# Kernel tuning notes

Measured on AMD Instinct MI355X. Metric: run time of the kernel, lower is better.

The kernel has to match this reference:

```python
import jax, jax.numpy as jnp
import numpy as np

NC1, NC2 = 97, 300   # EPIC-Kitchens verb / noun class counts
T_FRAMES = 24000     # frames in one long video
N_ACTIONS = 3806     # (verb, noun) action pairs in mapping.txt
HID = 512            # cfg.hid_dim


def setup_inputs() -> dict:
    key = jax.random.key(0)
    k1, k2, k3 = jax.random.split(key, 3)
    H = HID + NC1 + NC2  # 909: hidden features with class logits appended
    frame_feature = jax.random.normal(k1, (T_FRAMES, 1, H), dtype=jnp.float32)
    vids = jax.random.randint(k2, (N_ACTIONS,), 0, NC1, dtype=jnp.int32)
    nids = jax.random.randint(k3, (N_ACTIONS,), 0, NC2, dtype=jnp.int32)
    return {"frame_feature": frame_feature, "vids": vids, "nids": nids}


def _combine_verb_noun(clogit, vids, nids):
    # combine_verb_noun_to_action with apply_log=True:
    # log_softmax verbs and nouns separately, gather per action id, add.
    vlog = jax.nn.log_softmax(clogit[..., :NC1], axis=-1)
    nlog = jax.nn.log_softmax(clogit[..., NC1:], axis=-1)
    return vlog[..., vids] + nlog[..., nids]


def reference(frame_feature, vids, nids):
    T = frame_feature.shape[0]
    # --- verb/noun softmax-gather-multiply combine (frame level) ---
    clogit = frame_feature[..., -NC1 - NC2:]                 # [T,1,NC1+NC2]
    frame_logp = _combine_verb_noun(clogit, vids, nids)      # [T,1,A]

    # --- parse_label: segment ids from per-frame argmax prediction ---
    pred = jnp.argmax(frame_logp[:, 0], axis=-1)             # [T]
    change = jnp.concatenate(
        [jnp.zeros((1,), jnp.int32), (pred[1:] != pred[:-1]).astype(jnp.int32)]
    )
    seg_id = jax.lax.stop_gradient(jnp.cumsum(change))       # [T], in [0, nseg)

    # --- TemporalDownsampleUpsample.feature_frame2seg: mean-pool per segment ---
    feat = frame_feature[:, 0]                               # [T,H]
    seg_sum = jax.ops.segment_sum(feat, seg_id, num_segments=T)
    cnt = jax.ops.segment_sum(jnp.ones((T, 1), feat.dtype), seg_id, num_segments=T)
    seg_feat = seg_sum / jnp.maximum(cnt, 1.0)               # [T,H] (padded segments)

    # segment-level verb/noun combine
    seg_logp = _combine_verb_noun(seg_feat[:, -NC1 - NC2:], vids, nids)  # [T,A]

    # --- feature_seg2frame: broadcast segment values back to frames ---
    s2f = seg_logp[seg_id]                                   # [T,A]
    return frame_logp + s2f[:, None, :]                      # [T,1,A]
```

## Files before the change

### kernel.cpp

```cpp
#include <hip/hip_runtime.h>
#include <math.h>

#define T_FRAMES 24000
#define NC1 97
#define NC2 300
#define NCC 397
#define NA 3806
#define NA_PAD 3808
#define H_DIM 909
#define COFF 512
#define SLG_STRIDE 400


__device__ __forceinline__ float waveMax(float v) {
#pragma unroll
    for (int off = 32; off > 0; off >>= 1) v = fmaxf(v, __shfl_xor(v, off));
    return v;
}

__device__ __forceinline__ float waveSum(float v) {
#pragma unroll
    for (int off = 32; off > 0; off >>= 1) v += __shfl_xor(v, off);
    return v;
}

__device__ __forceinline__ unsigned flip32(float f) {
    unsigned u = __float_as_uint(f);
    return (u & 0x80000000u) ? ~u : (u | 0x80000000u);
}


__global__ __launch_bounds__(256) void k_pack(const int* __restrict__ vids,
                                              const int* __restrict__ nids,
                                              int* __restrict__ pk) {
    int a = blockIdx.x * 256 + threadIdx.x;
    if (a < NA_PAD) pk[a] = (a < NA) ? (vids[a] | (nids[a] << 16)) : 0;
}


__global__ __launch_bounds__(256) void k_frame(const float* __restrict__ ff,
                                               const int* __restrict__ pk,
                                               float2* __restrict__ fstats,
                                               int* __restrict__ pred) {
    const int tid = threadIdx.x;
    const int wid = tid >> 6, lane = tid & 63;
    const int t = blockIdx.x * 4 + wid;

    __shared__ float sh[4][SLG_STRIDE];
    float* S = sh[wid];

    const float* row = ff + (size_t)t * H_DIM + COFF;

    float xv[7];
    float vmax = -INFINITY, nmax = -INFINITY;
#pragma unroll
    for (int j = 0; j < 7; j++) {
        const int idx = lane + j * 64;
        float x = -INFINITY;
        if (idx < NCC) { x = row[idx]; S[idx] = x; }
        xv[j] = x;
        if (idx < NC1) vmax = fmaxf(vmax, x);
        else           nmax = fmaxf(nmax, x);
    }
    vmax = waveMax(vmax);
    nmax = waveMax(nmax);

    float vs = 0.f, ns = 0.f;
#pragma unroll
    for (int j = 0; j < 7; j++) {
        const int idx = lane + j * 64;
        if (idx < NC1)      vs += __expf(xv[j] - vmax);
        else if (idx < NCC) ns += __expf(xv[j] - nmax);
    }
    vs = waveSum(vs);
    ns = waveSum(ns);
    const float c1 = vmax + __logf(vs);
    const float c2 = nmax + __logf(ns);

    const int4* pk4 = (const int4*)pk;
    unsigned long long best = 0ull;
    for (int g = lane; g < NA_PAD / 4; g += 64) {
        const int4 p4 = pk4[g];
        const int pv[4] = {p4.x, p4.y, p4.z, p4.w};
#pragma unroll
        for (int j = 0; j < 4; j++) {
            const int a = g * 4 + j;
            if (a < NA) {
                const int p = pv[j];
                const float val = S[p & 0xffff] + S[NC1 + (p >> 16)];
                const unsigned long long key =
                    ((unsigned long long)flip32(val) << 32) | (unsigned)(~(unsigned)a);
                best = (key > best) ? key : best;
            }
        }
    }
#pragma unroll
    for (int off = 32; off > 0; off >>= 1) {
        unsigned long long o = __shfl_xor(best, off);
        best = (o > best) ? o : best;
    }

    if (lane == 0) {
        pred[t] = (int)(~(unsigned)best);
        fstats[t] = make_float2(c1, c2);
    }
}


__global__ __launch_bounds__(1024) void k_scan(const int* __restrict__ pred,
                                               int* __restrict__ seg_id,
                                               int* __restrict__ seg_start,
                                               int* __restrict__ Scount) {
    const int tid = threadIdx.x;
    __shared__ unsigned short sid16[T_FRAMES];
    __shared__ int wsum[16];

    for (int t = tid; t < T_FRAMES; t += 1024) {
        int chg = (t > 0) ? (pred[t] != pred[t - 1]) : 0;
        sid16[t] = (unsigned short)chg;
    }
    __syncthreads();

    const int CH = (T_FRAMES + 1023) / 1024;
    const int base = tid * CH;
    int cnt = 0;
    for (int k = 0; k < CH; k++) {
        int t = base + k;
        if (t < T_FRAMES) cnt += sid16[t];
    }
    const int lane = tid & 63, wid = tid >> 6;
    int inc = cnt;
#pragma unroll
    for (int d = 1; d < 64; d <<= 1) {
        int n = __shfl_up(inc, d);
        if (lane >= d) inc += n;
    }
    if (lane == 63) wsum[wid] = inc;
    __syncthreads();
    if (tid == 0) {
        int acc = 0;
        for (int i = 0; i < 16; i++) { int x = wsum[i]; wsum[i] = acc; acc += x; }
    }
    __syncthreads();
    int sid = wsum[wid] + inc - cnt;

    for (int k = 0; k < CH; k++) {
        int t = base + k;
        if (t >= T_FRAMES) break;
        if (t == 0) {
            seg_start[0] = 0;
        } else if (sid16[t]) {
            sid++;
            seg_start[sid] = t;
        }
        sid16[t] = (unsigned short)sid;
        if (t == T_FRAMES - 1) *Scount = sid + 1;
    }
    __syncthreads();

    for (int t = tid; t < T_FRAMES; t += 1024) seg_id[t] = (int)sid16[t];
}


__global__ __launch_bounds__(256) void k_seg(const float* __restrict__ ff,
                                             const int* __restrict__ seg_start,
                                             const int* __restrict__ Scount,
                                             float* __restrict__ seg_lg) {
    const int tid = threadIdx.x;
    const int wid = tid >> 6, lane = tid & 63;
    const int s = blockIdx.x * 4 + wid;
    const int S = *Scount;
    if (s >= S) return;

    const int start = seg_start[s];
    const int end = (s + 1 < S) ? seg_start[s + 1] : T_FRAMES;
    const int len = end - start;

    float acc[7] = {0.f, 0.f, 0.f, 0.f, 0.f, 0.f, 0.f};
    const float* basep = ff + (size_t)start * H_DIM + COFF;
    for (int k = 0; k < len; k++) {
        const float* p = basep + (size_t)k * H_DIM;
#pragma unroll
        for (int j = 0; j < 7; j++) {
            const int idx = lane + j * 64;
            if (idx < NCC) acc[j] += p[idx];
        }
    }
    const float inv = 1.f / (float)len;

    float xv[7];
    float vmax = -INFINITY, nmax = -INFINITY;
#pragma unroll
    for (int j = 0; j < 7; j++) {
        const int idx = lane + j * 64;
        float x = (idx < NCC) ? acc[j] * inv : -INFINITY;
        xv[j] = x;
        if (idx < NC1) vmax = fmaxf(vmax, x);
        else           nmax = fmaxf(nmax, x);
    }
    vmax = waveMax(vmax);
    nmax = waveMax(nmax);

    float vs = 0.f, ns = 0.f;
#pragma unroll
    for (int j = 0; j < 7; j++) {
        const int idx = lane + j * 64;
        if (idx < NC1)      vs += __expf(xv[j] - vmax);
        else if (idx < NCC) ns += __expf(xv[j] - nmax);
    }
    vs = waveSum(vs);
    ns = waveSum(ns);
    const float lv = __logf(vs), ln_ = __logf(ns);

    float* dst = seg_lg + (size_t)s * SLG_STRIDE;
#pragma unroll
    for (int j = 0; j < 7; j++) {
        const int idx = lane + j * 64;
        if (idx < NCC)
            dst[idx] = (idx < NC1) ? ((xv[j] - vmax) - lv) : ((xv[j] - nmax) - ln_);
    }
}


__global__ __launch_bounds__(256) void k_out(const float* __restrict__ ff,
                                             const int* __restrict__ pk,
                                             const float2* __restrict__ fstats,
                                             const int* __restrict__ seg_id,
                                             const float* __restrict__ seg_lg,
                                             float* __restrict__ out) {
    const int tid = threadIdx.x;
    const int wid = tid >> 6, lane = tid & 63;
    const int t = blockIdx.x * 4 + wid;

    __shared__ float sh[4][SLG_STRIDE];
    float* S = sh[wid];

    const int s = seg_id[t];
    const float2 c = fstats[t];
    const float* row = ff + (size_t)t * H_DIM + COFF;
    const float* srow = seg_lg + (size_t)s * SLG_STRIDE;

#pragma unroll
    for (int j = 0; j < 7; j++) {
        const int idx = lane + j * 64;
        if (idx < NCC)
            S[idx] = row[idx] + srow[idx] - ((idx < NC1) ? c.x : c.y);
    }

    const int2* pk2 = (const int2*)pk;
    float* orow = out + (size_t)t * NA;
    for (int g = lane; g < NA / 2; g += 64) {
        const int2 p2 = pk2[g];
        float2 o;
        o.x = S[p2.x & 0xffff] + S[NC1 + (p2.x >> 16)];
        o.y = S[p2.y & 0xffff] + S[NC1 + (p2.y >> 16)];
        *(float2*)(orow + 2 * g) = o;
    }
}


extern "C" void kernel_launch(void* const* d_in, const int* in_sizes, int n_in,
                              void* d_out, int out_size, void* d_ws, size_t ws_size,
                              hipStream_t stream) {
    const float* ff = (const float*)d_in[0];
    const int* vids = (const int*)d_in[1];
    const int* nids = (const int*)d_in[2];
    float* out = (float*)d_out;

    char* ws = (char*)d_ws;
    size_t off = 0;
    float2* fstats = (float2*)(ws + off); off += (size_t)T_FRAMES * 8;
    int* pred = (int*)(ws + off);         off += (size_t)T_FRAMES * 4;
    int* seg_id = (int*)(ws + off);       off += (size_t)T_FRAMES * 4;
    int* seg_start = (int*)(ws + off);    off += (size_t)T_FRAMES * 4;
    int* Scount = (int*)(ws + off);       off += 16;
    int* pk = (int*)(ws + off);           off += (size_t)NA_PAD * 4;
    float* seg_lg = (float*)(ws + off);   off += (size_t)T_FRAMES * SLG_STRIDE * 4;

    k_pack<<<(NA_PAD + 255) / 256, 256, 0, stream>>>(vids, nids, pk);
    k_frame<<<T_FRAMES / 4, 256, 0, stream>>>(ff, pk, fstats, pred);
    k_scan<<<1, 1024, 0, stream>>>(pred, seg_id, seg_start, Scount);
    k_seg<<<T_FRAMES / 4, 256, 0, stream>>>(ff, seg_start, Scount, seg_lg);
    k_out<<<T_FRAMES / 4, 256, 0, stream>>>(ff, pk, fstats, seg_id, seg_lg, out);
}
```

Before: 551.0 us.

## Fuse segment pooling with output writes and sort action keys by noun

Result: faster. 521.3 us (-5.4%).

```diff
diff --git a/kernel.cpp b/kernel.cpp
--- a/kernel.cpp
+++ b/kernel.cpp
@@ -7,9 +7,10 @@
 #define NCC 397
 #define NA 3806
 #define NA_PAD 3808
+#define NSORT 4096
 #define H_DIM 909
 #define COFF 512
-#define SLG_STRIDE 400
+#define TAB 400
 
 
 __device__ __forceinline__ float waveMax(float v) {
@@ -30,23 +31,59 @@
 }
 
 
-__global__ __launch_bounds__(256) void k_pack(const int* __restrict__ vids,
+__global__ __launch_bounds__(256) void k_prep(const int* __restrict__ vids,
                                               const int* __restrict__ nids,
-                                              int* __restrict__ pk) {
-    int a = blockIdx.x * 256 + threadIdx.x;
-    if (a < NA_PAD) pk[a] = (a < NA) ? (vids[a] | (nids[a] << 16)) : 0;
+                                              int* __restrict__ pk,
+                                              unsigned* __restrict__ skey) {
+    __shared__ unsigned cnt[NC2];
+    __shared__ unsigned ofs[NC2];
+    const int tid = threadIdx.x;
+
+    for (int i = tid; i < NC2; i += 256) cnt[i] = 0u;
+    __syncthreads();
+
+    for (int a = tid; a < NA; a += 256) {
+        int v = vids[a], n = nids[a];
+        pk[a] = v | (n << 16);
+        atomicAdd(&cnt[n], 1u);
+    }
+    __syncthreads();
+
+    if (tid < 64) {
+        unsigned run = 0;
+        for (int c = 0; c < 5; c++) {
+            int i = c * 64 + tid;
+            unsigned x = (i < NC2) ? cnt[i] : 0u;
+            unsigned inc = x;
+#pragma unroll
+            for (int d = 1; d < 64; d <<= 1) {
+                unsigned y = __shfl_up(inc, d);
+                if (tid >= d) inc += y;
+            }
+            if (i < NC2) ofs[i] = run + inc - x;
+            run += __shfl(inc, 63);
+        }
+    }
+    __syncthreads();
+
+    for (int a = tid; a < NA; a += 256) {
+        unsigned v = (unsigned)vids[a], n = (unsigned)nids[a];
+        unsigned p = atomicAdd(&ofs[n], 1u);
+        skey[p] = (n << 19) | (v << 12) | (unsigned)a;
+    }
+    for (int i = NA + tid; i < NSORT; i += 256) skey[i] = 0xFFFFFFFFu;
 }
 
 
 __global__ __launch_bounds__(256) void k_frame(const float* __restrict__ ff,
-                                               const int* __restrict__ pk,
+                                               const unsigned* __restrict__ skey,
                                                float2* __restrict__ fstats,
                                                int* __restrict__ pred) {
     const int tid = threadIdx.x;
     const int wid = tid >> 6, lane = tid & 63;
     const int t = blockIdx.x * 4 + wid;
 
-    __shared__ float sh[4][SLG_STRIDE];
+    __shared__ float sh[4][TAB];
     float* S = sh[wid];
 
     const float* row = ff + (size_t)t * H_DIM + COFF;
@@ -77,20 +114,19 @@
     const float c1 = vmax + __logf(vs);
     const float c2 = nmax + __logf(ns);
 
-    const int4* pk4 = (const int4*)pk;
+    const uint4* sk4 = (const uint4*)skey;
     unsigned long long best = 0ull;
-    for (int g = lane; g < NA_PAD / 4; g += 64) {
-        const int4 p4 = pk4[g];
-        const int pv[4] = {p4.x, p4.y, p4.z, p4.w};
+    for (int g = lane; g < NSORT / 4; g += 64) {
+        const uint4 kq = sk4[g];
+        const unsigned ks[4] = {kq.x, kq.y, kq.z, kq.w};
 #pragma unroll
         for (int j = 0; j < 4; j++) {
-            const int a = g * 4 + j;
-            if (a < NA) {
-                const int p = pv[j];
-                const float val = S[p & 0xffff] + S[NC1 + (p >> 16)];
-                const unsigned long long key =
-                    ((unsigned long long)flip32(val) << 32) | (unsigned)(~(unsigned)a);
-                best = (key > best) ? key : best;
+            const unsigned kk = ks[j];
+            if (kk != 0xFFFFFFFFu) {
+                const float val = S[(kk >> 12) & 0x7Fu] + S[NC1 + (kk >> 19)];
+                const unsigned long long rk =
+                    ((unsigned long long)flip32(val) << 32) | ((~kk) & 0xFFFu);
+                best = (rk > best) ? rk : best;
             }
         }
     }
@@ -101,24 +137,21 @@
     }
 
     if (lane == 0) {
-        pred[t] = (int)(~(unsigned)best);
+        pred[t] = (int)((~(unsigned)best) & 0xFFFu);
         fstats[t] = make_float2(c1, c2);
     }
 }
 
 
 __global__ __launch_bounds__(1024) void k_scan(const int* __restrict__ pred,
-                                               int* __restrict__ seg_id,
                                                int* __restrict__ seg_start,
                                                int* __restrict__ Scount) {
     const int tid = threadIdx.x;
-    __shared__ unsigned short sid16[T_FRAMES];
+    __shared__ unsigned short flg[T_FRAMES];
     __shared__ int wsum[16];
 
-    for (int t = tid; t < T_FRAMES; t += 1024) {
-        int chg = (t > 0) ? (pred[t] != pred[t - 1]) : 0;
-        sid16[t] = (unsigned short)chg;
-    }
+    for (int t = tid; t < T_FRAMES; t += 1024)
+        flg[t] = (unsigned short)((t > 0) ? (pred[t] != pred[t - 1]) : 0);
     __syncthreads();
 
     const int CH = (T_FRAMES + 1023) / 1024;
@@ -126,7 +159,7 @@
     int cnt = 0;
     for (int k = 0; k < CH; k++) {
         int t = base + k;
-        if (t < T_FRAMES) cnt += sid16[t];
+        if (t < T_FRAMES) cnt += flg[t];
     }
     const int lane = tid & 63, wid = tid >> 6;
     int inc = cnt;
@@ -147,25 +180,19 @@
     for (int k = 0; k < CH; k++) {
         int t = base + k;
         if (t >= T_FRAMES) break;
-        if (t == 0) {
-            seg_start[0] = 0;
-        } else if (sid16[t]) {
-            sid++;
-            seg_start[sid] = t;
-        }
-        sid16[t] = (unsigned short)sid;
+        if (t == 0) seg_start[0] = 0;
+        else if (flg[t]) { sid++; seg_start[sid] = t; }
         if (t == T_FRAMES - 1) *Scount = sid + 1;
     }
-    __syncthreads();
-
-    for (int t = tid; t < T_FRAMES; t += 1024) seg_id[t] = (int)sid16[t];
-}
-
-
-__global__ __launch_bounds__(256) void k_seg(const float* __restrict__ ff,
-                                             const int* __restrict__ seg_start,
-                                             const int* __restrict__ Scount,
-                                             float* __restrict__ seg_lg) {
+}
+
+
+__global__ __launch_bounds__(256) void k_segout(const float* __restrict__ ff,
+                                                const int* __restrict__ pk,
+                                                const float2* __restrict__ fstats,
+                                                const int* __restrict__ seg_start,
+                                                const int* __restrict__ Scount,
+                                                float* __restrict__ out) {
     const int tid = threadIdx.x;
     const int wid = tid >> 6, lane = tid & 63;
     const int s = blockIdx.x * 4 + wid;
@@ -173,7 +200,8 @@
     if (s >= S) return;
 
     const int start = seg_start[s];
-    const int end = (s + 1 < S) ? seg_start[s + 1] : T_FRAMES;
+    int end = (s + 1 < S) ? seg_start[s + 1] : T_FRAMES;
+    if (end > T_FRAMES) end = T_FRAMES;
     const int len = end - start;
 
     float acc[7] = {0.f, 0.f, 0.f, 0.f, 0.f, 0.f, 0.f};
@@ -188,73 +216,56 @@
     }
     const float inv = 1.f / (float)len;
 
-    float xv[7];
+    float lp[7];
     float vmax = -INFINITY, nmax = -INFINITY;
 #pragma unroll
     for (int j = 0; j < 7; j++) {
         const int idx = lane + j * 64;
         float x = (idx < NCC) ? acc[j] * inv : -INFINITY;
-        xv[j] = x;
+        lp[j] = x;
         if (idx < NC1) vmax = fmaxf(vmax, x);
         else           nmax = fmaxf(nmax, x);
     }
     vmax = waveMax(vmax);
     nmax = waveMax(nmax);
-
     float vs = 0.f, ns = 0.f;
 #pragma unroll
     for (int j = 0; j < 7; j++) {
         const int idx = lane + j * 64;
-        if (idx < NC1)      vs += __expf(xv[j] - vmax);
-        else if (idx < NCC) ns += __expf(xv[j] - nmax);
+        if (idx < NC1)      vs += __expf(lp[j] - vmax);
+        else if (idx < NCC) ns += __expf(lp[j] - nmax);
     }
     vs = waveSum(vs);
     ns = waveSum(ns);
-    const float lv = __logf(vs), ln_ = __logf(ns);
-
-    float* dst = seg_lg + (size_t)s * SLG_STRIDE;
-#pragma unroll
-    for (int j = 0; j < 7; j++) {
-        const int idx = lane + j * 64;
-        if (idx < NCC)
-            dst[idx] = (idx < NC1) ? ((xv[j] - vmax) - lv) : ((xv[j] - nmax) - ln_);
-    }
-}
-
-
-__global__ __launch_bounds__(256) void k_out(const float* __restrict__ ff,
-                                             const int* __restrict__ pk,
-                                             const float2* __restrict__ fstats,
-                                             const int* __restrict__ seg_id,
-                                             const float* __restrict__ seg_lg,
-                                             float* __restrict__ out) {
-    const int tid = threadIdx.x;
-    const int wid = tid >> 6, lane = tid & 63;
-    const int t = blockIdx.x * 4 + wid;
-
-    __shared__ float sh[4][SLG_STRIDE];
-    float* S = sh[wid];
-
-    const int s = seg_id[t];
-    const float2 c = fstats[t];
-    const float* row = ff + (size_t)t * H_DIM + COFF;
-    const float* srow = seg_lg + (size_t)s * SLG_STRIDE;
-
-#pragma unroll
-    for (int j = 0; j < 7; j++) {
-        const int idx = lane + j * 64;
-        if (idx < NCC)
-            S[idx] = row[idx] + srow[idx] - ((idx < NC1) ? c.x : c.y);
-    }
-
+    const float cv = vmax + __logf(vs);
+    const float cn = nmax + __logf(ns);
+#pragma unroll
+    for (int j = 0; j < 7; j++) {
+        const int idx = lane + j * 64;
+        lp[j] -= (idx < NC1) ? cv : cn;
+    }
+
+    __shared__ float sh[4][TAB];
+    float* Stab = sh[wid];
     const int2* pk2 = (const int2*)pk;
-    float* orow = out + (size_t)t * NA;
-    for (int g = lane; g < NA / 2; g += 64) {
-        const int2 p2 = pk2[g];
-        float2 o;
-        o.x = S[p2.x & 0xffff] + S[NC1 + (p2.x >> 16)];
-        o.y = S[p2.y & 0xffff] + S[NC1 + (p2.y >> 16)];
-        *(float2*)(orow + 2 * g) = o;
+
+    for (int t = start; t < end; t++) {
+        const float2 c = fstats[t];
+        const float* row = ff + (size_t)t * H_DIM + COFF;
+#pragma unroll
+        for (int j = 0; j < 7; j++) {
+            const int idx = lane + j * 64;
+            if (idx < NCC)
+                Stab[idx] = row[idx] + lp[j] - ((idx < NC1) ? c.x : c.y);
+        }
+        float* orow = out + (size_t)t * NA;
+        for (int g = lane; g < NA / 2; g += 64) {
+            const int2 p2 = pk2[g];
+            float2 o;
+            o.x = Stab[p2.x & 0xffff] + Stab[NC1 + (p2.x >> 16)];
+            o.y = Stab[p2.y & 0xffff] + Stab[NC1 + (p2.y >> 16)];
+            *(float2*)(orow + 2 * g) = o;
+        }
     }
 }
 
@@ -269,17 +280,15 @@
 
     char* ws = (char*)d_ws;
     size_t off = 0;
-    float2* fstats = (float2*)(ws + off); off += (size_t)T_FRAMES * 8;
-    int* pred = (int*)(ws + off);         off += (size_t)T_FRAMES * 4;
-    int* seg_id = (int*)(ws + off);       off += (size_t)T_FRAMES * 4;
-    int* seg_start = (int*)(ws + off);    off += (size_t)T_FRAMES * 4;
-    int* Scount = (int*)(ws + off);       off += 16;
-    int* pk = (int*)(ws + off);           off += (size_t)NA_PAD * 4;
-    float* seg_lg = (float*)(ws + off);   off += (size_t)T_FRAMES * SLG_STRIDE * 4;
-
-    k_pack<<<(NA_PAD + 255) / 256, 256, 0, stream>>>(vids, nids, pk);
-    k_frame<<<T_FRAMES / 4, 256, 0, stream>>>(ff, pk, fstats, pred);
-    k_scan<<<1, 1024, 0, stream>>>(pred, seg_id, seg_start, Scount);
-    k_seg<<<T_FRAMES / 4, 256, 0, stream>>>(ff, seg_start, Scount, seg_lg);
-    k_out<<<T_FRAMES / 4, 256, 0, stream>>>(ff, pk, fstats, seg_id, seg_lg, out);
-}
+    float2* fstats = (float2*)(ws + off);  off += (size_t)T_FRAMES * 8;
+    int* pred = (int*)(ws + off);          off += (size_t)T_FRAMES * 4;
+    int* seg_start = (int*)(ws + off);     off += (size_t)T_FRAMES * 4;
+    int* Scount = (int*)(ws + off);        off += 16;
+    int* pk = (int*)(ws + off);            off += (size_t)NA_PAD * 4;
+    unsigned* skey = (unsigned*)(ws + off); off += (size_t)NSORT * 4;
+
+    k_prep<<<1, 256, 0, stream>>>(vids, nids, pk, skey);
+    k_frame<<<T_FRAMES / 4, 256, 0, stream>>>(ff, skey, fstats, pred);
+    k_scan<<<1, 1024, 0, stream>>>(pred, seg_start, Scount);
+    k_segout<<<T_FRAMES / 4, 256, 0, stream>>>(ff, pk, fstats, seg_start, Scount, out);
+}
```
